# Kernel tuning notes

Hardware: AMD Instinct MI355X
Metric: run time of the kernel (lower is better)

The kernel has to match this reference:

```python
import jax, jax.numpy as jnp
import numpy as np

MASK_FRAC = 0.95  # fraction of zero-labeled attributes to drop per row


def setup_inputs() -> dict:
    key = jax.random.key(0)
    k1, k2 = jax.random.split(key)
    B, C = 8192, 1024
    scores = jax.random.normal(k1, (B, C), dtype=jnp.float32)
    attributes = jax.random.randint(k2, (B, C), 0, 2, dtype=jnp.int32)
    return {"scores": scores, "attributes": attributes}


def reference(scores, attributes):
    # scores: [B, C] float logits; attributes: [B, C] binary {0,1} labels
    B, C = scores.shape
    attrs = attributes.astype(scores.dtype)

    # Per-row: randomly zero out round(0.95 * n_zeros) of the zero-label
    # positions (without replacement). Vectorized: give each zero position a
    # uniform key, nonzero positions a sentinel > 1, rank within the row, and
    # drop the k smallest ranks (all of which are zero positions).
    is_zero = attrs == 0
    u = jax.random.uniform(jax.random.key(42), (B, C))
    u = jnp.where(is_zero, u, 2.0)
    ranks = jnp.argsort(jnp.argsort(u, axis=1), axis=1)  # [B, C] rank of each pos
    n_zero = is_zero.sum(axis=1)  # [B]
    k = jnp.round(n_zero.astype(jnp.float32) * MASK_FRAC).astype(jnp.int32)  # [B]
    loss_mask = jnp.where(ranks < k[:, None], 0.0, 1.0).astype(scores.dtype)

    # multilabel_soft_margin_loss with per-class weight, mean over classes,
    # then mean over batch (original sums per-row losses and divides by B).
    ls_pos = jax.nn.log_sigmoid(scores)
    ls_neg = jax.nn.log_sigmoid(-scores)
    per_elem = loss_mask * (attrs * ls_pos + (1.0 - attrs) * ls_neg)  # [B, C]
    per_row = -per_elem.mean(axis=1)  # [B]
    return per_row.mean()
```

## Files before the change

kernel.cpp:

```cpp
#include <hip/hip_runtime.h>
#include <stdint.h>

static constexpr int B_ROWS = 8192;
static constexpr int C_COLS = 1024;
static constexpr uint32_t HALF_N = 4194304u;
static constexpr int NPAIR = B_ROWS / 2;

__device__ __forceinline__ uint32_t rotl32(uint32_t x, int d) {
  return (x << d) | (x >> (32 - d));
}

__device__ __forceinline__ void threefry2x32_k42(uint32_t& x0, uint32_t& x1) {
  const uint32_t ks0 = 0u;
  const uint32_t ks1 = 42u;
  const uint32_t ks2 = 0u ^ 42u ^ 0x1BD11BDAu;
  x0 += ks0; x1 += ks1;
#define TF_R(r) { x0 += x1; x1 = rotl32(x1, (r)); x1 ^= x0; }
  TF_R(13) TF_R(15) TF_R(26) TF_R(6)
  x0 += ks1; x1 += ks2 + 1u;
  TF_R(17) TF_R(29) TF_R(16) TF_R(24)
  x0 += ks2; x1 += ks0 + 2u;
  TF_R(13) TF_R(15) TF_R(26) TF_R(6)
  x0 += ks0; x1 += ks1 + 3u;
  TF_R(17) TF_R(29) TF_R(16) TF_R(24)
  x0 += ks1; x1 += ks2 + 4u;
  TF_R(13) TF_R(15) TF_R(26) TF_R(6)
  x0 += ks2; x1 += ks0 + 5u;
#undef TF_R
}

__device__ __forceinline__ int wave_iscan_add(int x) {
  x += __builtin_amdgcn_update_dpp(0, x, 0x111, 0xf, 0xf, false);
  x += __builtin_amdgcn_update_dpp(0, x, 0x112, 0xf, 0xf, false);
  x += __builtin_amdgcn_update_dpp(0, x, 0x114, 0xf, 0xf, false);
  x += __builtin_amdgcn_update_dpp(0, x, 0x118, 0xf, 0xf, false);
  x += __builtin_amdgcn_update_dpp(0, x, 0x142, 0xa, 0xf, false);
  x += __builtin_amdgcn_update_dpp(0, x, 0x143, 0xc, 0xf, false);
  return x;
}

__device__ __forceinline__ uint32_t wave_min_u32(uint32_t x) {
  uint32_t t;
#define MSTEP(ctrl, rmask)                                                   \
  t = (uint32_t)__builtin_amdgcn_update_dpp(-1, (int)x, ctrl, rmask, 0xf, false); \
  x = (t < x) ? t : x;
  MSTEP(0x111, 0xf) MSTEP(0x112, 0xf) MSTEP(0x114, 0xf) MSTEP(0x118, 0xf)
  MSTEP(0x142, 0xa) MSTEP(0x143, 0xc)
#undef MSTEP
  return x;
}

__device__ __forceinline__ int wave_max_i32(int x) {
  int t;
#define XSTEP(ctrl, rmask)                                                   \
  t = __builtin_amdgcn_update_dpp(-1, x, ctrl, rmask, 0xf, false);           \
  x = (t > x) ? t : x;
  XSTEP(0x111, 0xf) XSTEP(0x112, 0xf) XSTEP(0x114, 0xf) XSTEP(0x118, 0xf)
  XSTEP(0x142, 0xa) XSTEP(0x143, 0xc)
#undef XSTEP
  return x;
}

__device__ __forceinline__ float wave_fadd(float x) {
#define FSTEP(ctrl, rmask)                                                   \
  x += __int_as_float(                                                       \
      __builtin_amdgcn_update_dpp(0, __float_as_int(x), ctrl, rmask, 0xf, false));
  FSTEP(0x111, 0xf) FSTEP(0x112, 0xf) FSTEP(0x114, 0xf) FSTEP(0x118, 0xf)
  FSTEP(0x142, 0xa) FSTEP(0x143, 0xc)
#undef FSTEP
  return x;
}

__global__ __launch_bounds__(128) void attr_loss_main(
    const float* __restrict__ scores, const int* __restrict__ attrs,
    float* __restrict__ partials) {
  __shared__ int hist[2][256];
  __shared__ uint32_t xbuf[2][512];

  const int t = threadIdx.x;
  const int lane = t & 63;
  const int w = t >> 6;
  const int pair = blockIdx.x;
  const int myrow = pair + w * NPAIR;
  const int selfc0 = w * 512 + lane * 8;
  const int othc0 = (1 - w) * 512 + lane * 8;

  const float* srow = scores + (size_t)myrow * C_COLS;
  const int* arow = attrs + (size_t)myrow * C_COLS;
  const int4 a0 = *reinterpret_cast<const int4*>(arow + selfc0);
  const int4 a1 = *reinterpret_cast<const int4*>(arow + selfc0 + 4);
  const int4 a2 = *reinterpret_cast<const int4*>(arow + othc0);
  const int4 a3 = *reinterpret_cast<const int4*>(arow + othc0 + 4);
  const float4 s0 = *reinterpret_cast<const float4*>(srow + selfc0);
  const float4 s1 = *reinterpret_cast<const float4*>(srow + selfc0 + 4);
  const float4 s2 = *reinterpret_cast<const float4*>(srow + othc0);
  const float4 s3 = *reinterpret_cast<const float4*>(srow + othc0 + 4);

  *reinterpret_cast<int4*>(&hist[w][lane * 4]) = make_int4(0, 0, 0, 0);

  uint32_t key[16];
#pragma unroll
  for (int j = 0; j < 8; ++j) {
    const int col = selfc0 + j;
    uint32_t x0 = (uint32_t)(pair * C_COLS + col);
    uint32_t x1 = x0 + HALF_N;
    threefry2x32_k42(x0, x1);
    const uint32_t cb = (uint32_t)col >> 1;
    const uint32_t k0 = (x0 & 0xFFFFFE00u) | cb;
    const uint32_t k1 = (x1 & 0xFFFFFE00u) | cb;
    key[j] = w ? k1 : k0;
    xbuf[w][j * 64 + lane] = w ? k0 : k1;
  }

  uint32_t zm = 0u;
  zm |= (a0.x == 0 ? 1u : 0u) << 0;  zm |= (a0.y == 0 ? 1u : 0u) << 1;
  zm |= (a0.z == 0 ? 1u : 0u) << 2;  zm |= (a0.w == 0 ? 1u : 0u) << 3;
  zm |= (a1.x == 0 ? 1u : 0u) << 4;  zm |= (a1.y == 0 ? 1u : 0u) << 5;
  zm |= (a1.z == 0 ? 1u : 0u) << 6;  zm |= (a1.w == 0 ? 1u : 0u) << 7;
  zm |= (a2.x == 0 ? 1u : 0u) << 8;  zm |= (a2.y == 0 ? 1u : 0u) << 9;
  zm |= (a2.z == 0 ? 1u : 0u) << 10; zm |= (a2.w == 0 ? 1u : 0u) << 11;
  zm |= (a3.x == 0 ? 1u : 0u) << 12; zm |= (a3.y == 0 ? 1u : 0u) << 13;
  zm |= (a3.z == 0 ? 1u : 0u) << 14; zm |= (a3.w == 0 ? 1u : 0u) << 15;

#pragma unroll
  for (int e = 0; e < 8; ++e) {
    atomicAdd(&hist[w][key[e] >> 24], (int)((zm >> e) & 1u));
  }

  __syncthreads();
#pragma unroll
  for (int j = 0; j < 8; ++j) key[8 + j] = xbuf[1 - w][j * 64 + lane];

#pragma unroll
  for (int e = 8; e < 16; ++e) {
    atomicAdd(&hist[w][key[e] >> 24], (int)((zm >> e) & 1u));
  }

  const int4 hv = *reinterpret_cast<const int4*>(&hist[w][lane * 4]);
  const int c0 = hv.x, c1 = c0 + hv.y, c2 = c1 + hv.z, c3 = c2 + hv.w;
  const int incl = wave_iscan_add(c3);
  const int excl = incl - c3;
  const int n_zero = __builtin_amdgcn_readlane(incl, 63);
  const int k = (int)rintf(0.95f * (float)n_zero);

  uint32_t T = 0u;
  if (k > 0) {
    const int target = k - 1;
    int enc = -1;
    const int ce0 = excl, ce1 = excl + c0, ce2 = excl + c1, ce3 = excl + c2;
    if (hv.x > 0 && ce0 <= target && target < ce0 + hv.x) enc = ((lane * 4 + 0) << 16) | (target - ce0);
    if (hv.y > 0 && ce1 <= target && target < ce1 + hv.y) enc = ((lane * 4 + 1) << 16) | (target - ce1);
    if (hv.z > 0 && ce2 <= target && target < ce2 + hv.z) enc = ((lane * 4 + 2) << 16) | (target - ce2);
    if (hv.w > 0 && ce3 <= target && target < ce3 + hv.w) enc = ((lane * 4 + 3) << 16) | (target - ce3);
    const int benc = __builtin_amdgcn_readlane(wave_max_i32(enc), 63);
    const uint32_t bucket = (uint32_t)(benc >> 16);
    int tt = benc & 0xFFFF;

    uint32_t lowbar = 0u;
    while (true) {
      uint32_t mm = 0xFFFFFFFFu;
#pragma unroll
      for (int e = 0; e < 16; ++e) {
        const uint32_t kv = key[e];
        const bool cand = ((zm >> e) & 1u) && ((kv >> 24) == bucket) && (kv >= lowbar);
        const uint32_t v = cand ? kv : 0xFFFFFFFFu;
        mm = mm < v ? mm : v;
      }
      const uint32_t gmin = (uint32_t)__builtin_amdgcn_readlane((int)wave_min_u32(mm), 63);
      int c = 0;
#pragma unroll
      for (int e = 0; e < 16; ++e)
        c += (((zm >> e) & 1u) && key[e] == gmin) ? 1 : 0;
      const int ctot = __builtin_amdgcn_readlane(wave_iscan_add(c), 63);
      if (tt < ctot) { T = gmin; break; }
      tt -= ctot;
      lowbar = gmin + 1u;
    }
  }

  const bool nodrops = (k <= 0);
  float lsum = 0.f;
#define LOSS_ELEM(sval, e)                                                   \
  {                                                                          \
    const float s = (sval);                                                  \
    const bool z = (zm >> (e)) & 1u;                                         \
    const float cmn = __logf(1.f + __expf(-fabsf(s)));                       \
    const float x = z ? -s : s;                                              \
    const bool keep = !z || nodrops || (key[(e)] > T);                       \
    lsum += keep ? (fminf(x, 0.f) - cmn) : 0.f;                              \
  }
  LOSS_ELEM(s0.x, 0)  LOSS_ELEM(s0.y, 1)  LOSS_ELEM(s0.z, 2)  LOSS_ELEM(s0.w, 3)
  LOSS_ELEM(s1.x, 4)  LOSS_ELEM(s1.y, 5)  LOSS_ELEM(s1.z, 6)  LOSS_ELEM(s1.w, 7)
  LOSS_ELEM(s2.x, 8)  LOSS_ELEM(s2.y, 9)  LOSS_ELEM(s2.z, 10) LOSS_ELEM(s2.w, 11)
  LOSS_ELEM(s3.x, 12) LOSS_ELEM(s3.y, 13) LOSS_ELEM(s3.z, 14) LOSS_ELEM(s3.w, 15)
#undef LOSS_ELEM

  lsum = wave_fadd(lsum);
  if (lane == 63) partials[blockIdx.x * 2 + w] = lsum;
}

__global__ __launch_bounds__(256) void finalize_kernel(
    const float* __restrict__ partials, float* __restrict__ out) {
  __shared__ double wred[4];
  const int t = threadIdx.x;
  const int lane = t & 63;
  const int w = t >> 6;
  double s = 0.0;
#pragma unroll
  for (int i = 0; i < 32; ++i) s += (double)partials[t + i * 256];
#pragma unroll
  for (int d = 32; d >= 1; d >>= 1) s += __shfl_xor(s, d, 64);
  if (lane == 0) wred[w] = s;
  __syncthreads();
  if (t == 0) {
    const double tot = wred[0] + wred[1] + wred[2] + wred[3];
    out[0] = (float)(-tot / ((double)B_ROWS * (double)C_COLS));
  }
}

extern "C" void kernel_launch(void* const* d_in, const int* in_sizes, int n_in,
                              void* d_out, int out_size, void* d_ws, size_t ws_size,
                              hipStream_t stream) {
  const float* scores = (const float*)d_in[0];
  const int* attrs = (const int*)d_in[1];
  float* out = (float*)d_out;
  float* partials = (float*)d_ws;

  attr_loss_main<<<NPAIR, 128, 0, stream>>>(scores, attrs, partials);
  finalize_kernel<<<1, 256, 0, stream>>>(partials, out);
}
```

Before: 103.2 us.

## Process two row pairs per block and prefetch next attributes

```diff
diff --git a/kernel.cpp b/kernel.cpp
--- a/kernel.cpp
+++ b/kernel.cpp
@@ -5,6 +5,8 @@
 static constexpr int C_COLS = 1024;
 static constexpr uint32_t HALF_N = 4194304u;
 static constexpr int NPAIR = B_ROWS / 2;
+static constexpr int PAIRS_PER_BLOCK = 2;
+static constexpr int GRID = NPAIR / PAIRS_PER_BLOCK;
 
 __device__ __forceinline__ uint32_t rotl32(uint32_t x, int d) {
   return (x << d) | (x >> (32 - d));
@@ -75,125 +77,143 @@
     const float* __restrict__ scores, const int* __restrict__ attrs,
     float* __restrict__ partials) {
   __shared__ int hist[2][256];
-  __shared__ uint32_t xbuf[2][512];
+  __shared__ uint32_t xbuf[2][2][512];
 
   const int t = threadIdx.x;
   const int lane = t & 63;
   const int w = t >> 6;
-  const int pair = blockIdx.x;
-  const int myrow = pair + w * NPAIR;
   const int selfc0 = w * 512 + lane * 8;
   const int othc0 = (1 - w) * 512 + lane * 8;
 
-  const float* srow = scores + (size_t)myrow * C_COLS;
-  const int* arow = attrs + (size_t)myrow * C_COLS;
-  const int4 a0 = *reinterpret_cast<const int4*>(arow + selfc0);
-  const int4 a1 = *reinterpret_cast<const int4*>(arow + selfc0 + 4);
-  const int4 a2 = *reinterpret_cast<const int4*>(arow + othc0);
-  const int4 a3 = *reinterpret_cast<const int4*>(arow + othc0 + 4);
-  const float4 s0 = *reinterpret_cast<const float4*>(srow + selfc0);
-  const float4 s1 = *reinterpret_cast<const float4*>(srow + selfc0 + 4);
-  const float4 s2 = *reinterpret_cast<const float4*>(srow + othc0);
-  const float4 s3 = *reinterpret_cast<const float4*>(srow + othc0 + 4);
-
-  *reinterpret_cast<int4*>(&hist[w][lane * 4]) = make_int4(0, 0, 0, 0);
-
-  uint32_t key[16];
-#pragma unroll
-  for (int j = 0; j < 8; ++j) {
-    const int col = selfc0 + j;
-    uint32_t x0 = (uint32_t)(pair * C_COLS + col);
-    uint32_t x1 = x0 + HALF_N;
-    threefry2x32_k42(x0, x1);
-    const uint32_t cb = (uint32_t)col >> 1;
-    const uint32_t k0 = (x0 & 0xFFFFFE00u) | cb;
-    const uint32_t k1 = (x1 & 0xFFFFFE00u) | cb;
-    key[j] = w ? k1 : k0;
-    xbuf[w][j * 64 + lane] = w ? k0 : k1;
+  int4 na0, na1, na2, na3;
+  {
+    const int* arow = attrs + (size_t)(blockIdx.x + w * NPAIR) * C_COLS;
+    na0 = *reinterpret_cast<const int4*>(arow + selfc0);
+    na1 = *reinterpret_cast<const int4*>(arow + selfc0 + 4);
+    na2 = *reinterpret_cast<const int4*>(arow + othc0);
+    na3 = *reinterpret_cast<const int4*>(arow + othc0 + 4);
   }
 
-  uint32_t zm = 0u;
-  zm |= (a0.x == 0 ? 1u : 0u) << 0;  zm |= (a0.y == 0 ? 1u : 0u) << 1;
-  zm |= (a0.z == 0 ? 1u : 0u) << 2;  zm |= (a0.w == 0 ? 1u : 0u) << 3;
-  zm |= (a1.x == 0 ? 1u : 0u) << 4;  zm |= (a1.y == 0 ? 1u : 0u) << 5;
-  zm |= (a1.z == 0 ? 1u : 0u) << 6;  zm |= (a1.w == 0 ? 1u : 0u) << 7;
-  zm |= (a2.x == 0 ? 1u : 0u) << 8;  zm |= (a2.y == 0 ? 1u : 0u) << 9;
-  zm |= (a2.z == 0 ? 1u : 0u) << 10; zm |= (a2.w == 0 ? 1u : 0u) << 11;
-  zm |= (a3.x == 0 ? 1u : 0u) << 12; zm |= (a3.y == 0 ? 1u : 0u) << 13;
-  zm |= (a3.z == 0 ? 1u : 0u) << 14; zm |= (a3.w == 0 ? 1u : 0u) << 15;
-
-#pragma unroll
-  for (int e = 0; e < 8; ++e) {
-    atomicAdd(&hist[w][key[e] >> 24], (int)((zm >> e) & 1u));
+  float lsum = 0.f;
+
+  for (int it = 0; it < PAIRS_PER_BLOCK; ++it) {
+    const int pair = blockIdx.x + it * GRID;
+    const int myrow = pair + w * NPAIR;
+
+    uint32_t zm = 0u;
+    zm |= (na0.x == 0 ? 1u : 0u) << 0;  zm |= (na0.y == 0 ? 1u : 0u) << 1;
+    zm |= (na0.z == 0 ? 1u : 0u) << 2;  zm |= (na0.w == 0 ? 1u : 0u) << 3;
+    zm |= (na1.x == 0 ? 1u : 0u) << 4;  zm |= (na1.y == 0 ? 1u : 0u) << 5;
+    zm |= (na1.z == 0 ? 1u : 0u) << 6;  zm |= (na1.w == 0 ? 1u : 0u) << 7;
+    zm |= (na2.x == 0 ? 1u : 0u) << 8;  zm |= (na2.y == 0 ? 1u : 0u) << 9;
+    zm |= (na2.z == 0 ? 1u : 0u) << 10; zm |= (na2.w == 0 ? 1u : 0u) << 11;
+    zm |= (na3.x == 0 ? 1u : 0u) << 12; zm |= (na3.y == 0 ? 1u : 0u) << 13;
+    zm |= (na3.z == 0 ? 1u : 0u) << 14; zm |= (na3.w == 0 ? 1u : 0u) << 15;
+
+    const float* srow = scores + (size_t)myrow * C_COLS;
+    const float4 s0 = *reinterpret_cast<const float4*>(srow + selfc0);
+    const float4 s1 = *reinterpret_cast<const float4*>(srow + selfc0 + 4);
+    const float4 s2 = *reinterpret_cast<const float4*>(srow + othc0);
+    const float4 s3 = *reinterpret_cast<const float4*>(srow + othc0 + 4);
+
+    if (it + 1 < PAIRS_PER_BLOCK) {
+      const int* arow =
+          attrs + (size_t)(blockIdx.x + (it + 1) * GRID + w * NPAIR) * C_COLS;
+      na0 = *reinterpret_cast<const int4*>(arow + selfc0);
+      na1 = *reinterpret_cast<const int4*>(arow + selfc0 + 4);
+      na2 = *reinterpret_cast<const int4*>(arow + othc0);
+      na3 = *reinterpret_cast<const int4*>(arow + othc0 + 4);
+    }
+
+    *reinterpret_cast<int4*>(&hist[w][lane * 4]) = make_int4(0, 0, 0, 0);
+
+    uint32_t key[16];
+#pragma unroll
+    for (int j = 0; j < 8; ++j) {
+      const int col = selfc0 + j;
+      uint32_t x0 = (uint32_t)(pair * C_COLS + col);
+      uint32_t x1 = x0 + HALF_N;
+      threefry2x32_k42(x0, x1);
+      const uint32_t cb = (uint32_t)col >> 1;
+      const uint32_t k0 = (x0 & 0xFFFFFE00u) | cb;
+      const uint32_t k1 = (x1 & 0xFFFFFE00u) | cb;
+      key[j] = w ? k1 : k0;
+      xbuf[w][it & 1][j * 64 + lane] = w ? k0 : k1;
+    }
+
+#pragma unroll
+    for (int e = 0; e < 8; ++e) {
+      atomicAdd(&hist[w][key[e] >> 24], (int)((zm >> e) & 1u));
+    }
+
+    __syncthreads();
+#pragma unroll
+    for (int j = 0; j < 8; ++j) key[8 + j] = xbuf[1 - w][it & 1][j * 64 + lane];
+
+#pragma unroll
+    for (int e = 8; e < 16; ++e) {
+      atomicAdd(&hist[w][key[e] >> 24], (int)((zm >> e) & 1u));
+    }
+
+    const int4 hv = *reinterpret_cast<const int4*>(&hist[w][lane * 4]);
+    const int c0 = hv.x, c1 = c0 + hv.y, c2 = c1 + hv.z, c3 = c2 + hv.w;
+    const int incl = wave_iscan_add(c3);
+    const int excl = incl - c3;
+    const int n_zero = __builtin_amdgcn_readlane(incl, 63);
+    const int k = (int)rintf(0.95f * (float)n_zero);
+
+    uint32_t T = 0u;
+    if (k > 0) {
+      const int target = k - 1;
+      int enc = -1;
+      const int ce0 = excl, ce1 = excl + c0, ce2 = excl + c1, ce3 = excl + c2;
+      if (hv.x > 0 && ce0 <= target && target < ce0 + hv.x) enc = ((lane * 4 + 0) << 16) | (target - ce0);
+      if (hv.y > 0 && ce1 <= target && target < ce1 + hv.y) enc = ((lane * 4 + 1) << 16) | (target - ce1);
+      if (hv.z > 0 && ce2 <= target && target < ce2 + hv.z) enc = ((lane * 4 + 2) << 16) | (target - ce2);
+      if (hv.w > 0 && ce3 <= target && target < ce3 + hv.w) enc = ((lane * 4 + 3) << 16) | (target - ce3);
+      const int benc = __builtin_amdgcn_readlane(wave_max_i32(enc), 63);
+      const uint32_t bucket = (uint32_t)(benc >> 16);
+      int tt = benc & 0xFFFF;
+
+      uint32_t lowbar = 0u;
+      while (true) {
+        uint32_t mm = 0xFFFFFFFFu;
+#pragma unroll
+        for (int e = 0; e < 16; ++e) {
+          const uint32_t kv = key[e];
+          const bool cand = ((zm >> e) & 1u) && ((kv >> 24) == bucket) && (kv >= lowbar);
+          const uint32_t v = cand ? kv : 0xFFFFFFFFu;
+          mm = mm < v ? mm : v;
+        }
+        const uint32_t gmin =
+            (uint32_t)__builtin_amdgcn_readlane((int)wave_min_u32(mm), 63);
+        int c = 0;
+#pragma unroll
+        for (int e = 0; e < 16; ++e)
+          c += (((zm >> e) & 1u) && key[e] == gmin) ? 1 : 0;
+        const int ctot = __builtin_amdgcn_readlane(wave_iscan_add(c), 63);
+        if (tt < ctot) { T = gmin; break; }
+        tt -= ctot;
+        lowbar = gmin + 1u;
+      }
+    }
+
+    const bool nodrops = (k <= 0);
+#define LOSS_ELEM(sval, e)                                                   \
+    {                                                                        \
+      const float s = (sval);                                                \
+      const bool z = (zm >> (e)) & 1u;                                       \
+      const float cmn = __logf(1.f + __expf(-fabsf(s)));                     \
+      const float x = z ? -s : s;                                            \
+      const bool keep = !z || nodrops || (key[(e)] > T);                     \
+      lsum += keep ? (fminf(x, 0.f) - cmn) : 0.f;                            \
+    }
+    LOSS_ELEM(s0.x, 0)  LOSS_ELEM(s0.y, 1)  LOSS_ELEM(s0.z, 2)  LOSS_ELEM(s0.w, 3)
+    LOSS_ELEM(s1.x, 4)  LOSS_ELEM(s1.y, 5)  LOSS_ELEM(s1.z, 6)  LOSS_ELEM(s1.w, 7)
+    LOSS_ELEM(s2.x, 8)  LOSS_ELEM(s2.y, 9)  LOSS_ELEM(s2.z, 10) LOSS_ELEM(s2.w, 11)
+    LOSS_ELEM(s3.x, 12) LOSS_ELEM(s3.y, 13) LOSS_ELEM(s3.z, 14) LOSS_ELEM(s3.w, 15)
+#undef LOSS_ELEM
   }
-
-  __syncthreads();
-#pragma unroll
-  for (int j = 0; j < 8; ++j) key[8 + j] = xbuf[1 - w][j * 64 + lane];
-
-#pragma unroll
-  for (int e = 8; e < 16; ++e) {
-    atomicAdd(&hist[w][key[e] >> 24], (int)((zm >> e) & 1u));
-  }
-
-  const int4 hv = *reinterpret_cast<const int4*>(&hist[w][lane * 4]);
-  const int c0 = hv.x, c1 = c0 + hv.y, c2 = c1 + hv.z, c3 = c2 + hv.w;
-  const int incl = wave_iscan_add(c3);
-  const int excl = incl - c3;
-  const int n_zero = __builtin_amdgcn_readlane(incl, 63);
-  const int k = (int)rintf(0.95f * (float)n_zero);
-
-  uint32_t T = 0u;
-  if (k > 0) {
-    const int target = k - 1;
-    int enc = -1;
-    const int ce0 = excl, ce1 = excl + c0, ce2 = excl + c1, ce3 = excl + c2;
-    if (hv.x > 0 && ce0 <= target && target < ce0 + hv.x) enc = ((lane * 4 + 0) << 16) | (target - ce0);
-    if (hv.y > 0 && ce1 <= target && target < ce1 + hv.y) enc = ((lane * 4 + 1) << 16) | (target - ce1);
-    if (hv.z > 0 && ce2 <= target && target < ce2 + hv.z) enc = ((lane * 4 + 2) << 16) | (target - ce2);
-    if (hv.w > 0 && ce3 <= target && target < ce3 + hv.w) enc = ((lane * 4 + 3) << 16) | (target - ce3);
-    const int benc = __builtin_amdgcn_readlane(wave_max_i32(enc), 63);
-    const uint32_t bucket = (uint32_t)(benc >> 16);
-    int tt = benc & 0xFFFF;
-
-    uint32_t lowbar = 0u;
-    while (true) {
-      uint32_t mm = 0xFFFFFFFFu;
-#pragma unroll
-      for (int e = 0; e < 16; ++e) {
-        const uint32_t kv = key[e];
-        const bool cand = ((zm >> e) & 1u) && ((kv >> 24) == bucket) && (kv >= lowbar);
-        const uint32_t v = cand ? kv : 0xFFFFFFFFu;
-        mm = mm < v ? mm : v;
-      }
-      const uint32_t gmin = (uint32_t)__builtin_amdgcn_readlane((int)wave_min_u32(mm), 63);
-      int c = 0;
-#pragma unroll
-      for (int e = 0; e < 16; ++e)
-        c += (((zm >> e) & 1u) && key[e] == gmin) ? 1 : 0;
-      const int ctot = __builtin_amdgcn_readlane(wave_iscan_add(c), 63);
-      if (tt < ctot) { T = gmin; break; }
-      tt -= ctot;
-      lowbar = gmin + 1u;
-    }
-  }
-
-  const bool nodrops = (k <= 0);
-  float lsum = 0.f;
-#define LOSS_ELEM(sval, e)                                                   \
-  {                                                                          \
-    const float s = (sval);                                                  \
-    const bool z = (zm >> (e)) & 1u;                                         \
-    const float cmn = __logf(1.f + __expf(-fabsf(s)));                       \
-    const float x = z ? -s : s;                                              \
-    const bool keep = !z || nodrops || (key[(e)] > T);                       \
-    lsum += keep ? (fminf(x, 0.f) - cmn) : 0.f;                              \
-  }
-  LOSS_ELEM(s0.x, 0)  LOSS_ELEM(s0.y, 1)  LOSS_ELEM(s0.z, 2)  LOSS_ELEM(s0.w, 3)
-  LOSS_ELEM(s1.x, 4)  LOSS_ELEM(s1.y, 5)  LOSS_ELEM(s1.z, 6)  LOSS_ELEM(s1.w, 7)
-  LOSS_ELEM(s2.x, 8)  LOSS_ELEM(s2.y, 9)  LOSS_ELEM(s2.z, 10) LOSS_ELEM(s2.w, 11)
-  LOSS_ELEM(s3.x, 12) LOSS_ELEM(s3.y, 13) LOSS_ELEM(s3.z, 14) LOSS_ELEM(s3.w, 15)
-#undef LOSS_ELEM
 
   lsum = wave_fadd(lsum);
   if (lane == 63) partials[blockIdx.x * 2 + w] = lsum;
@@ -207,7 +227,7 @@
   const int w = t >> 6;
   double s = 0.0;
 #pragma unroll
-  for (int i = 0; i < 32; ++i) s += (double)partials[t + i * 256];
+  for (int i = 0; i < 16; ++i) s += (double)partials[t + i * 256];
 #pragma unroll
   for (int d = 32; d >= 1; d >>= 1) s += __shfl_xor(s, d, 64);
   if (lane == 0) wred[w] = s;
@@ -226,6 +246,6 @@
   float* out = (float*)d_out;
   float* partials = (float*)d_ws;
 
-  attr_loss_main<<<NPAIR, 128, 0, stream>>>(scores, attrs, partials);
+  attr_loss_main<<<GRID, 128, 0, stream>>>(scores, attrs, partials);
   finalize_kernel<<<1, 256, 0, stream>>>(partials, out);
 }
```

Result: slower. 109.7 us (+6.3%).
